# Kernel optimization log

Hardware: AMD Instinct MI355X
Metric: run time of the kernel (lower is better)

Reference implementation:

```python
import jax, jax.numpy as jnp
import numpy as np
from math import log2, ceil

NUM_LEAVES = 128
KERNEL = 8
STRIDE = 8
PADDING = 0
LR = 0.3

LEAF_NUM = 2 ** ceil(log2(NUM_LEAVES))   # 128
DEPTH = int(log2(LEAF_NUM))              # 7
NUM_NODES = 2 * LEAF_NUM - 1             # 255


def _ancestor_table():
    # A[j-1, t-1] = global heap index of the ancestor of node j at tree level t,
    # or -1 if t exceeds j's own level. Nodes use heap indexing: children of i
    # are 2i+1, 2i+2 (matches the layer bookkeeping in the torch module).
    A = np.full((NUM_NODES - 1, DEPTH), -1, dtype=np.int32)
    for j in range(1, NUM_NODES):
        lvl = int(np.floor(np.log2(j + 1)))
        anc = j
        for t in range(lvl, 0, -1):
            A[j - 1, t - 1] = anc
            anc = (anc - 1) // 2
    return jnp.asarray(A)

_ANC = _ancestor_table()  # (NUM_NODES-1, DEPTH)


def img2patches(x):
    x = jnp.pad(x, PADDING)
    H, W = x.shape
    n0 = (H - KERNEL) // STRIDE + 1
    n1 = (W - KERNEL) // STRIDE + 1
    win = jnp.arange(KERNEL)
    rows = jnp.arange(n0)[:, None] * STRIDE + win[None, :]  # (n0, k)
    cols = jnp.arange(n1)[:, None] * STRIDE + win[None, :]  # (n1, k)
    p = x[rows[:, None, :, None], cols[None, :, None, :]]   # (n0, n1, k, k)
    return p.reshape(n0 * n1, KERNEL * KERNEL)


def setup_inputs() -> dict:
    key = jax.random.key(0)
    k1, k2 = jax.random.split(key)
    image = jax.random.uniform(k1, (2048, 2048), dtype=jnp.float32)
    nodes = jax.random.uniform(k2, (NUM_NODES, KERNEL * KERNEL), dtype=jnp.float32)
    return {"image": image, "nodes": nodes}


def reference(image, nodes):
    X = img2patches(image)                      # (P, k^2)
    P = X.shape[0]

    # --- hierarchical BMU descent (binary tree, DEPTH levels) ---
    cur = jnp.zeros((P,), dtype=jnp.int32)      # root
    bmu_levels = []
    for _ in range(DEPTH):
        c0 = 2 * cur + 1
        c1 = 2 * cur + 2
        # pnorm with p=2 in the source is (sum((a-b)^2))^2 -- monotone, kept faithful
        d0 = jnp.sum((nodes[c0] - X) ** 2, axis=-1) ** 2
        d1 = jnp.sum((nodes[c1] - X) ** 2, axis=-1) ** 2
        cur = jnp.where(d1 < d0, c1, c0)        # tie -> first (c0), like torch.min
        bmu_levels.append(cur)
    bmu_path = jnp.stack(bmu_levels, axis=1)    # (P, DEPTH), bmu at levels 1..DEPTH

    # --- layer_state for every non-root node: number of levels at which the
    # node's ancestor coincides with the BMU chain (== the torch concatenated
    # layer_state, columns ordered by global node index 1..NUM_NODES-1) ---
    state = jnp.sum(_ANC[None, :, :] == bmu_path[:, None, :], axis=-1)  # (P, N-1)

    lrates = LR * (2.0 ** jnp.arange(1, DEPTH + 2, dtype=jnp.float32)) / 2.0 ** (DEPTH + 1)
    lrs = lrates[state]                          # (P, N-1)

    # mean_p lrs[p,j] * (X[p,:] - nodes[1+j,:])
    #   = (lrs^T @ X)/P - mean_p(lrs)[:,None] * nodes[1:]
    upd = jnp.einsum('pj,pk->jk', lrs, X) / P - lrs.mean(axis=0)[:, None] * nodes[1:]
    new_nodes = nodes.at[1:].add(upd)

    return new_nodes, cur[:, None]               # updated codebook, leaf BMU per patch
```

## Files before the change

kernel.cpp:

```cpp
#include <hip/hip_runtime.h>

#define IMG_W 2048
#define NUM_NODES 255
#define NLEAF 128
#define DEPTH 7
#define RS 68

template<int CTRL>
__device__ __forceinline__ float dpp_add(float x) {
    int v = __builtin_amdgcn_update_dpp(0, __float_as_int(x), CTRL, 0xF, 0xF, true);
    return x + __int_as_float(v);
}
__device__ __forceinline__ float group16_sum(float x) {
    x = dpp_add<0xB1>(x);
    x = dpp_add<0x4E>(x);
    x = dpp_add<0x141>(x);
    x = dpp_add<0x128>(x);
    return x;
}

__global__ __launch_bounds__(1024, 4) void fusedK(const float* __restrict__ img,
                                                  const float* __restrict__ nodes,
                                                  float* __restrict__ leaf_out,
                                                  float* __restrict__ S,
                                                  unsigned* __restrict__ cnt)
{
    __shared__ float nds[NUM_NODES * RS];
    __shared__ float Sl[NLEAF * RS];
    __shared__ unsigned cntl[NLEAF];

    const int t = threadIdx.x;
    const int b = blockIdx.x;
    const int g = t >> 4;
    const int q = t & 15;
    const int q4 = q * 4;

    for (int i = t; i < NLEAF * RS; i += 1024) Sl[i] = 0.0f;
    if (t < NLEAF) cntl[t] = 0u;

    const float4* ng = (const float4*)nodes;
    for (int i = t; i < NUM_NODES * 16; i += 1024) {
        *(float4*)&nds[(i >> 4) * RS + (i & 15) * 4] = ng[i];
    }

    float4 xv0, xv1, xv2, xv3;
    {
        const int roff = (q >> 1), coff = (q & 1) * 4;
        int p = b * 256 + g;
        xv0 = *(const float4*)(img + (size_t)((p >> 8) * 8 + roff) * IMG_W + (p & 255) * 8 + coff);
        p += 64;
        xv1 = *(const float4*)(img + (size_t)((p >> 8) * 8 + roff) * IMG_W + (p & 255) * 8 + coff);
        p += 64;
        xv2 = *(const float4*)(img + (size_t)((p >> 8) * 8 + roff) * IMG_W + (p & 255) * 8 + coff);
        p += 64;
        xv3 = *(const float4*)(img + (size_t)((p >> 8) * 8 + roff) * IMG_W + (p & 255) * 8 + coff);
    }
    __syncthreads();

    int cur0 = 0, cur1 = 0, cur2 = 0, cur3 = 0;
    #pragma unroll
    for (int lvl = 0; lvl < DEPTH; ++lvl) {
        const int ca = 2 * cur0 + 1;
        const int cb = 2 * cur1 + 1;
        const int cc = 2 * cur2 + 1;
        const int cd = 2 * cur3 + 1;
        const float* pa = &nds[ca * RS + q4];
        const float* pb = &nds[cb * RS + q4];
        const float* pc = &nds[cc * RS + q4];
        const float* pd = &nds[cd * RS + q4];
        const float4 A0 = *(const float4*)(pa);
        const float4 B0 = *(const float4*)(pa + RS);
        const float4 A1 = *(const float4*)(pb);
        const float4 B1 = *(const float4*)(pb + RS);
        const float4 A2 = *(const float4*)(pc);
        const float4 B2 = *(const float4*)(pc + RS);
        const float4 A3 = *(const float4*)(pd);
        const float4 B3 = *(const float4*)(pd + RS);

        float d, s0, s1;
        s0 = 0.f; s1 = 0.f;
        d = A0.x - xv0.x; s0 = fmaf(d, d, s0);  d = B0.x - xv0.x; s1 = fmaf(d, d, s1);
        d = A0.y - xv0.y; s0 = fmaf(d, d, s0);  d = B0.y - xv0.y; s1 = fmaf(d, d, s1);
        d = A0.z - xv0.z; s0 = fmaf(d, d, s0);  d = B0.z - xv0.z; s1 = fmaf(d, d, s1);
        d = A0.w - xv0.w; s0 = fmaf(d, d, s0);  d = B0.w - xv0.w; s1 = fmaf(d, d, s1);
        cur0 = (group16_sum(s1 - s0) < 0.0f) ? (ca + 1) : ca;
        s0 = 0.f; s1 = 0.f;
        d = A1.x - xv1.x; s0 = fmaf(d, d, s0);  d = B1.x - xv1.x; s1 = fmaf(d, d, s1);
        d = A1.y - xv1.y; s0 = fmaf(d, d, s0);  d = B1.y - xv1.y; s1 = fmaf(d, d, s1);
        d = A1.z - xv1.z; s0 = fmaf(d, d, s0);  d = B1.z - xv1.z; s1 = fmaf(d, d, s1);
        d = A1.w - xv1.w; s0 = fmaf(d, d, s0);  d = B1.w - xv1.w; s1 = fmaf(d, d, s1);
        cur1 = (group16_sum(s1 - s0) < 0.0f) ? (cb + 1) : cb;
        s0 = 0.f; s1 = 0.f;
        d = A2.x - xv2.x; s0 = fmaf(d, d, s0);  d = B2.x - xv2.x; s1 = fmaf(d, d, s1);
        d = A2.y - xv2.y; s0 = fmaf(d, d, s0);  d = B2.y - xv2.y; s1 = fmaf(d, d, s1);
        d = A2.z - xv2.z; s0 = fmaf(d, d, s0);  d = B2.z - xv2.z; s1 = fmaf(d, d, s1);
        d = A2.w - xv2.w; s0 = fmaf(d, d, s0);  d = B2.w - xv2.w; s1 = fmaf(d, d, s1);
        cur2 = (group16_sum(s1 - s0) < 0.0f) ? (cc + 1) : cc;
        s0 = 0.f; s1 = 0.f;
        d = A3.x - xv3.x; s0 = fmaf(d, d, s0);  d = B3.x - xv3.x; s1 = fmaf(d, d, s1);
        d = A3.y - xv3.y; s0 = fmaf(d, d, s0);  d = B3.y - xv3.y; s1 = fmaf(d, d, s1);
        d = A3.z - xv3.z; s0 = fmaf(d, d, s0);  d = B3.z - xv3.z; s1 = fmaf(d, d, s1);
        d = A3.w - xv3.w; s0 = fmaf(d, d, s0);  d = B3.w - xv3.w; s1 = fmaf(d, d, s1);
        cur3 = (group16_sum(s1 - s0) < 0.0f) ? (cd + 1) : cd;
    }

    if (q == 0) {
        leaf_out[b * 256 + g]       = (float)cur0;
        leaf_out[b * 256 + 64 + g]  = (float)cur1;
        leaf_out[b * 256 + 128 + g] = (float)cur2;
        leaf_out[b * 256 + 192 + g] = (float)cur3;
        atomicAdd(&cntl[cur0 - 127], 1u);
        atomicAdd(&cntl[cur1 - 127], 1u);
        atomicAdd(&cntl[cur2 - 127], 1u);
        atomicAdd(&cntl[cur3 - 127], 1u);
    }

    {
        float* dst = &Sl[(cur0 - 127) * RS + q4];
        atomicAdd(dst + 0, xv0.x); atomicAdd(dst + 1, xv0.y);
        atomicAdd(dst + 2, xv0.z); atomicAdd(dst + 3, xv0.w);
        dst = &Sl[(cur1 - 127) * RS + q4];
        atomicAdd(dst + 0, xv1.x); atomicAdd(dst + 1, xv1.y);
        atomicAdd(dst + 2, xv1.z); atomicAdd(dst + 3, xv1.w);
        dst = &Sl[(cur2 - 127) * RS + q4];
        atomicAdd(dst + 0, xv2.x); atomicAdd(dst + 1, xv2.y);
        atomicAdd(dst + 2, xv2.z); atomicAdd(dst + 3, xv2.w);
        dst = &Sl[(cur3 - 127) * RS + q4];
        atomicAdd(dst + 0, xv3.x); atomicAdd(dst + 1, xv3.y);
        atomicAdd(dst + 2, xv3.z); atomicAdd(dst + 3, xv3.w);
    }
    __syncthreads();

    for (int i = t; i < NLEAF * 64; i += 1024) {
        const float v = Sl[(i >> 6) * RS + (i & 63)];
        if (v != 0.0f) atomicAdd(&S[i], v);
    }
    if (t < NLEAF && cntl[t] != 0u) atomicAdd(&cnt[t], cntl[t]);
}

__global__ __launch_bounds__(256) void updateK(const float* __restrict__ nodes,
                                               const float* __restrict__ S,
                                               const unsigned* __restrict__ cnt,
                                               float* __restrict__ out)
{
    const int gid = blockIdx.x * 256 + threadIdx.x;
    if (gid >= NUM_NODES * 64) return;
    const int n = gid >> 6, k = gid & 63;
    const float nd = nodes[gid];
    if (n == 0) { out[gid] = nd; return; }

    const int pos = n + 1;
    const int Ln = 31 - __clz(pos);
    float su = 0.f, sc = 0.f;
    #pragma unroll 8
    for (int L = 0; L < NLEAF; ++L) {
        const int a = (128 + L) >> (7 - Ln);
        const int x = pos ^ a;
        const int state = (x == 0) ? Ln : (Ln - (31 - __clz(x)) - 1);
        const float lr = 0.3f * ((float)(1 << state) * (1.0f / 128.0f));
        su = fmaf(lr, S[L * 64 + k], su);
        sc = fmaf(lr, (float)cnt[L], sc);
    }
    const float invP = 1.0f / 65536.0f;
    out[gid] = nd + su * invP - (sc * invP) * nd;
}

extern "C" void kernel_launch(void* const* d_in, const int* in_sizes, int n_in,
                              void* d_out, int out_size, void* d_ws, size_t ws_size,
                              hipStream_t stream)
{
    const float* img   = (const float*)d_in[0];
    const float* nodes = (const float*)d_in[1];

    float* out_nodes = (float*)d_out;
    float* out_leaf  = out_nodes + NUM_NODES * 64;

    float*    S   = (float*)d_ws;
    unsigned* cnt = (unsigned*)(S + NLEAF * 64);

    hipMemsetAsync(d_ws, 0, (NLEAF * 64) * sizeof(float) + NLEAF * sizeof(unsigned), stream);
    fusedK<<<256, 1024, 0, stream>>>(img, nodes, out_leaf, S, cnt);
    updateK<<<64, 256, 0, stream>>>(nodes, S, cnt, out_nodes);
}
```

Before: 108.5 us.

## Replace shared-memory float atomics with counting-sort segmented leaf accumulation

Instead of each thread atomically adding patch values into a per-block shared leaf-sum array, the kernel records each patch's leaf, prefix-sums the leaf counts, bucket-sorts patch indices, and has each thread sum its leaf's patches serially before one global atomic per leaf/column. Patches are staged in the node buffer after the descent. The block is also halved to 512 threads with 128 patches each, and the grid is doubled. This removes LDS float atomic contention and the zeroing/flush of a large shared array, but adds several barriers, a scan, and serial per-leaf loops.

```diff
diff --git a/kernel.cpp b/kernel.cpp
--- a/kernel.cpp
+++ b/kernel.cpp
@@ -5,6 +5,7 @@
 #define NLEAF 128
 #define DEPTH 7
 #define RS 68
+#define NPATCH 128
 
 template<int CTRL>
 __device__ __forceinline__ float dpp_add(float x) {
@@ -19,15 +20,19 @@
     return x;
 }
 
-__global__ __launch_bounds__(1024, 4) void fusedK(const float* __restrict__ img,
-                                                  const float* __restrict__ nodes,
-                                                  float* __restrict__ leaf_out,
-                                                  float* __restrict__ S,
-                                                  unsigned* __restrict__ cnt)
+__global__ __launch_bounds__(512, 4) void fusedK(const float* __restrict__ img,
+                                                 const float* __restrict__ nodes,
+                                                 float* __restrict__ leaf_out,
+                                                 float* __restrict__ S,
+                                                 unsigned* __restrict__ cnt)
 {
     __shared__ float nds[NUM_NODES * RS];
-    __shared__ float Sl[NLEAF * RS];
-    __shared__ unsigned cntl[NLEAF];
+    __shared__ int   Lbuf[NPATCH];
+    __shared__ int   pos[NLEAF + 1];
+    __shared__ int   curp[NLEAF];
+    __shared__ int   sortedIdx[NPATCH];
+    __shared__ int   cntl[NLEAF];
+    float* XN = nds;
 
     const int t = threadIdx.x;
     const int b = blockIdx.x;
@@ -35,24 +40,23 @@
     const int q = t & 15;
     const int q4 = q * 4;
 
-    for (int i = t; i < NLEAF * RS; i += 1024) Sl[i] = 0.0f;
-    if (t < NLEAF) cntl[t] = 0u;
+    if (t < NLEAF) cntl[t] = 0;
 
     const float4* ng = (const float4*)nodes;
-    for (int i = t; i < NUM_NODES * 16; i += 1024) {
+    for (int i = t; i < NUM_NODES * 16; i += 512) {
         *(float4*)&nds[(i >> 4) * RS + (i & 15) * 4] = ng[i];
     }
 
     float4 xv0, xv1, xv2, xv3;
     {
         const int roff = (q >> 1), coff = (q & 1) * 4;
-        int p = b * 256 + g;
+        int p = b * NPATCH + g;
         xv0 = *(const float4*)(img + (size_t)((p >> 8) * 8 + roff) * IMG_W + (p & 255) * 8 + coff);
-        p += 64;
+        p += 32;
         xv1 = *(const float4*)(img + (size_t)((p >> 8) * 8 + roff) * IMG_W + (p & 255) * 8 + coff);
-        p += 64;
+        p += 32;
         xv2 = *(const float4*)(img + (size_t)((p >> 8) * 8 + roff) * IMG_W + (p & 255) * 8 + coff);
-        p += 64;
+        p += 32;
         xv3 = *(const float4*)(img + (size_t)((p >> 8) * 8 + roff) * IMG_W + (p & 255) * 8 + coff);
     }
     __syncthreads();
@@ -60,10 +64,7 @@
     int cur0 = 0, cur1 = 0, cur2 = 0, cur3 = 0;
     #pragma unroll
     for (int lvl = 0; lvl < DEPTH; ++lvl) {
-        const int ca = 2 * cur0 + 1;
-        const int cb = 2 * cur1 + 1;
-        const int cc = 2 * cur2 + 1;
-        const int cd = 2 * cur3 + 1;
+        const int ca = 2 * cur0 + 1, cb = 2 * cur1 + 1, cc = 2 * cur2 + 1, cd = 2 * cur3 + 1;
         const float* pa = &nds[ca * RS + q4];
         const float* pb = &nds[cb * RS + q4];
         const float* pc = &nds[cc * RS + q4];
@@ -105,37 +106,61 @@
     }
 
     if (q == 0) {
-        leaf_out[b * 256 + g]       = (float)cur0;
-        leaf_out[b * 256 + 64 + g]  = (float)cur1;
-        leaf_out[b * 256 + 128 + g] = (float)cur2;
-        leaf_out[b * 256 + 192 + g] = (float)cur3;
-        atomicAdd(&cntl[cur0 - 127], 1u);
-        atomicAdd(&cntl[cur1 - 127], 1u);
-        atomicAdd(&cntl[cur2 - 127], 1u);
-        atomicAdd(&cntl[cur3 - 127], 1u);
-    }
-
-    {
-        float* dst = &Sl[(cur0 - 127) * RS + q4];
-        atomicAdd(dst + 0, xv0.x); atomicAdd(dst + 1, xv0.y);
-        atomicAdd(dst + 2, xv0.z); atomicAdd(dst + 3, xv0.w);
-        dst = &Sl[(cur1 - 127) * RS + q4];
-        atomicAdd(dst + 0, xv1.x); atomicAdd(dst + 1, xv1.y);
-        atomicAdd(dst + 2, xv1.z); atomicAdd(dst + 3, xv1.w);
-        dst = &Sl[(cur2 - 127) * RS + q4];
-        atomicAdd(dst + 0, xv2.x); atomicAdd(dst + 1, xv2.y);
-        atomicAdd(dst + 2, xv2.z); atomicAdd(dst + 3, xv2.w);
-        dst = &Sl[(cur3 - 127) * RS + q4];
-        atomicAdd(dst + 0, xv3.x); atomicAdd(dst + 1, xv3.y);
-        atomicAdd(dst + 2, xv3.z); atomicAdd(dst + 3, xv3.w);
-    }
-    __syncthreads();
-
-    for (int i = t; i < NLEAF * 64; i += 1024) {
-        const float v = Sl[(i >> 6) * RS + (i & 63)];
-        if (v != 0.0f) atomicAdd(&S[i], v);
-    }
-    if (t < NLEAF && cntl[t] != 0u) atomicAdd(&cnt[t], cntl[t]);
+        leaf_out[b * NPATCH + g]      = (float)cur0;
+        leaf_out[b * NPATCH + 32 + g] = (float)cur1;
+        leaf_out[b * NPATCH + 64 + g] = (float)cur2;
+        leaf_out[b * NPATCH + 96 + g] = (float)cur3;
+        Lbuf[g]      = cur0 - 127;
+        Lbuf[32 + g] = cur1 - 127;
+        Lbuf[64 + g] = cur2 - 127;
+        Lbuf[96 + g] = cur3 - 127;
+        atomicAdd(&cntl[cur0 - 127], 1);
+        atomicAdd(&cntl[cur1 - 127], 1);
+        atomicAdd(&cntl[cur2 - 127], 1);
+        atomicAdd(&cntl[cur3 - 127], 1);
+    }
+    __syncthreads();
+
+    *(float4*)&XN[(g)      * RS + q4] = xv0;
+    *(float4*)&XN[(32 + g) * RS + q4] = xv1;
+    *(float4*)&XN[(64 + g) * RS + q4] = xv2;
+    *(float4*)&XN[(96 + g) * RS + q4] = xv3;
+
+    if (t == 0) pos[0] = 0;
+    if (t < NLEAF) pos[t + 1] = cntl[t];
+    __syncthreads();
+    for (int st = 1; st <= NLEAF; st <<= 1) {
+        int v = 0;
+        if (t <= NLEAF && t >= st) v = pos[t - st];
+        __syncthreads();
+        if (t <= NLEAF && t >= st) pos[t] += v;
+        __syncthreads();
+    }
+    if (t < NLEAF) curp[t] = pos[t];
+    __syncthreads();
+
+    if (q == 0) {
+        int i0 = atomicAdd(&curp[Lbuf[g]], 1);       sortedIdx[i0] = g;
+        int i1 = atomicAdd(&curp[Lbuf[32 + g]], 1);  sortedIdx[i1] = 32 + g;
+        int i2 = atomicAdd(&curp[Lbuf[64 + g]], 1);  sortedIdx[i2] = 64 + g;
+        int i3 = atomicAdd(&curp[Lbuf[96 + g]], 1);  sortedIdx[i3] = 96 + g;
+    }
+    __syncthreads();
+
+    const int w = t >> 6, k = t & 63;
+    #pragma unroll
+    for (int r = 0; r < 16; ++r) {
+        const int L = w * 16 + r;
+        const int s = pos[L], e = pos[L + 1];
+        if (e > s) {
+            float acc = 0.0f;
+            for (int i = s; i < e; ++i) {
+                acc += XN[sortedIdx[i] * RS + k];
+            }
+            atomicAdd(&S[L * 64 + k], acc);
+            if (k == 0) atomicAdd(&cnt[L], (unsigned)(e - s));
+        }
+    }
 }
 
 __global__ __launch_bounds__(256) void updateK(const float* __restrict__ nodes,
@@ -179,6 +204,6 @@
     unsigned* cnt = (unsigned*)(S + NLEAF * 64);
 
     hipMemsetAsync(d_ws, 0, (NLEAF * 64) * sizeof(float) + NLEAF * sizeof(unsigned), stream);
-    fusedK<<<256, 1024, 0, stream>>>(img, nodes, out_leaf, S, cnt);
+    fusedK<<<512, 512, 0, stream>>>(img, nodes, out_leaf, S, cnt);
     updateK<<<64, 256, 0, stream>>>(nodes, S, cnt, out_nodes);
 }
```

Result: slower. 178.1 us (+64.1%).
